# Optimization experiments

Measured on AMD Instinct MI355X. Metric: run time of the kernel, lower is better.

## Reference

```python
import jax, jax.numpy as jnp
import numpy as np

IN_DIM = 128
SLOT_SIZE = 64
NUM_SLOTS = 8
NUM_ITERS = 3
MLP_HDIM = 128
EPSILON = 1e-08


def _layernorm(x, g, b, eps=1e-5):
    m = jnp.mean(x, axis=-1, keepdims=True)
    v = jnp.mean((x - m) ** 2, axis=-1, keepdims=True)
    return (x - m) * jax.lax.rsqrt(v + eps) * g + b


def setup_inputs() -> dict:
    key = jax.random.key(0)
    ks = jax.random.split(key, 16)
    H, D, K, M = SLOT_SIZE, IN_DIM, NUM_SLOTS, MLP_HDIM
    x = jax.random.normal(ks[0], (32, 4096, D), dtype=jnp.float32)
    noise = jax.random.normal(ks[1], (32, K, H), dtype=jnp.float32)
    s = lambda k, shape, fan_in: jax.random.normal(k, shape, jnp.float32) * (1.0 / np.sqrt(fan_in))
    return {
        'x': x,
        'noise': noise,
        'Wq': s(ks[2], (H, H), H),            # project_q (no bias)
        'Wk': s(ks[3], (H, D), D),            # project_k
        'Wv': s(ks[4], (H, D), D),            # project_v
        'ln_in_g': jnp.ones((D,), jnp.float32), 'ln_in_b': jnp.zeros((D,), jnp.float32),
        'ln_sl_g': jnp.ones((H,), jnp.float32), 'ln_sl_b': jnp.zeros((H,), jnp.float32),
        'ln_mlp_g': jnp.ones((H,), jnp.float32), 'ln_mlp_b': jnp.zeros((H,), jnp.float32),
        'gru_w_ih': s(ks[5], (3 * H, H), H),  # PyTorch GRUCell weight_ih (r,z,n)
        'gru_w_hh': s(ks[6], (3 * H, H), H),
        'gru_b_ih': jnp.zeros((3 * H,), jnp.float32),
        'gru_b_hh': jnp.zeros((3 * H,), jnp.float32),
        'mlp_w1': s(ks[7], (M, H), H), 'mlp_b1': jnp.zeros((M,), jnp.float32),
        'mlp_w2': s(ks[8], (H, M), M), 'mlp_b2': jnp.zeros((H,), jnp.float32),
        'slots_mu': jnp.tile(jnp.linspace(-1.0, 1.0, K, dtype=jnp.float32)[None, :, None], (1, 1, H)),
        'slots_logsigma': jnp.full((1, K, H), -1.0, dtype=jnp.float32),
    }


def reference(x, noise, Wq, Wk, Wv, ln_in_g, ln_in_b, ln_sl_g, ln_sl_b,
              ln_mlp_g, ln_mlp_b, gru_w_ih, gru_w_hh, gru_b_ih, gru_b_hh,
              mlp_w1, mlp_b1, mlp_w2, mlp_b2, slots_mu, slots_logsigma):
    B = x.shape[0]
    H, K = SLOT_SIZE, NUM_SLOTS
    xn = _layernorm(x, ln_in_g, ln_in_b)
    k = jnp.einsum('bnd,hd->bnh', xn, Wk)  # [B,N,H]
    v = jnp.einsum('bnd,hd->bnh', xn, Wv)

    scale = jax.nn.softplus(slots_logsigma) + 1e-05
    slots = slots_mu + scale * noise  # rsample, broadcast over batch -> [B,K,H]

    def step(slots):
        slots_prev = slots
        s = _layernorm(slots, ln_sl_g, ln_sl_b)
        q = jnp.einsum('bkh,gh->bkg', s, Wq)  # [B,K,H]
        scores = (H ** -0.5) * jnp.einsum('bnh,bkh->bnk', k, q)
        attn = jax.nn.softmax(scores, axis=-1) + EPSILON  # softmax over slots
        attn = attn / jnp.sum(attn, axis=1, keepdims=True)  # normalize over inputs
        updates = jnp.einsum('bnk,bnh->bkh', attn, v)
        # PyTorch GRUCell: gates ordered (r, z, n)
        u = updates.reshape(-1, H)
        h = slots_prev.reshape(-1, H)
        gx = u @ gru_w_ih.T + gru_b_ih
        gh = h @ gru_w_hh.T + gru_b_hh
        xr, xz, xn_ = jnp.split(gx, 3, axis=-1)
        hr, hz, hn = jnp.split(gh, 3, axis=-1)
        r = jax.nn.sigmoid(xr + hr)
        z = jax.nn.sigmoid(xz + hz)
        n = jnp.tanh(xn_ + r * hn)
        slots = ((1.0 - z) * n + z * h).reshape(B, K, H)
        slots = _layernorm(slots, ln_mlp_g, ln_mlp_b)
        mlp_out = jax.nn.relu(slots @ mlp_w1.T + mlp_b1) @ mlp_w2.T + mlp_b2
        return slots + mlp_out

    for _ in range(NUM_ITERS):
        slots = step(slots)
    return slots
```

## Files before the change

kernel.cpp:

```cpp
#include <hip/hip_runtime.h>

typedef __attribute__((ext_vector_type(8))) short s16x8;
typedef __attribute__((ext_vector_type(4))) float f32x4;

#define DEV static __device__ __forceinline__

DEV float b2f(unsigned short u){
  unsigned int i = ((unsigned int)u) << 16;
  float f; __builtin_memcpy(&f, &i, 4); return f;
}
DEV unsigned short f2b(float f){
  unsigned int i; __builtin_memcpy(&i, &f, 4);
  i = i + 0x7fffu + ((i >> 16) & 1u);
  return (unsigned short)(i >> 16);
}
DEV f32x4 mfma16(s16x8 a, s16x8 b, f32x4 c){
  return __builtin_amdgcn_mfma_f32_16x16x32_bf16(a, b, c, 0, 0, 0);
}
DEV s16x8 ld8f(const float* p){
  const float4* q4 = (const float4*)p;
  float4 a = q4[0], b = q4[1];
  s16x8 r;
  r[0]=(short)f2b(a.x); r[1]=(short)f2b(a.y); r[2]=(short)f2b(a.z); r[3]=(short)f2b(a.w);
  r[4]=(short)f2b(b.x); r[5]=(short)f2b(b.y); r[6]=(short)f2b(b.z); r[7]=(short)f2b(b.w);
  return r;
}

__global__ __launch_bounds__(256) void k_lnkv(
    const float* __restrict__ x,
    const float* __restrict__ Wk,
    const float* __restrict__ Wv,
    const float* __restrict__ lg,
    const float* __restrict__ lb,
    unsigned short* __restrict__ kg,
    unsigned short* __restrict__ vt)
{
  __shared__ unsigned int xs[128 * 68];
  const int tid = threadIdx.x;
  const int w = tid >> 6, ln = tid & 63;
  const int m16 = ln & 15, q = ln >> 4;
  const int b = blockIdx.x >> 5;
  const int nbase = (blockIdx.x & 31) << 7;
  const long rowg0 = (long)b * 4096 + nbase;

  {
    const int half = ln >> 5;
    const int L = ln & 31;
    const float4 gl4 = *(const float4*)(lg + L*4);
    const float4 bl4 = *(const float4*)(lb + L*4);
    for (int i = 0; i < 16; i += 4){
      float4 xv[4];
      #pragma unroll
      for (int j = 0; j < 4; ++j){
        int r = w*32 + (i+j)*2 + half;
        xv[j] = *(const float4*)(x + (rowg0 + r)*128 + L*4);
      }
      #pragma unroll
      for (int j = 0; j < 4; ++j){
        int r = w*32 + (i+j)*2 + half;
        float4 v = xv[j];
        float s1 = v.x + v.y + v.z + v.w;
        float s2 = v.x*v.x + v.y*v.y + v.z*v.z + v.w*v.w;
        #pragma unroll
        for (int m = 16; m >= 1; m >>= 1){
          s1 += __shfl_xor(s1, m);
          s2 += __shfl_xor(s2, m);
        }
        float mean = s1 * (1.f/128.f);
        float var  = s2 * (1.f/128.f) - mean*mean;
        float rs = rsqrtf(var + 1e-5f);
        float y0 = (v.x - mean)*rs*gl4.x + bl4.x;
        float y1 = (v.y - mean)*rs*gl4.y + bl4.y;
        float y2 = (v.z - mean)*rs*gl4.z + bl4.z;
        float y3 = (v.w - mean)*rs*gl4.w + bl4.w;
        uint2 pk;
        pk.x = (unsigned int)f2b(y0) | ((unsigned int)f2b(y1) << 16);
        pk.y = (unsigned int)f2b(y2) | ((unsigned int)f2b(y3) << 16);
        *(uint2*)&xs[r*68 + L*2] = pk;
      }
    }
  }
  __syncthreads();

  s16x8 bw[4][8];
  #pragma unroll
  for (int nt = 0; nt < 8; ++nt){
    const float* Wp = (nt < 4) ? (Wk + (nt*16 + m16)*128)
                               : (Wv + ((nt-4)*16 + m16)*128);
    #pragma unroll
    for (int kb = 0; kb < 4; ++kb)
      bw[kb][nt] = ld8f(Wp + kb*32 + q*8);
  }

  const f32x4 zf = {0.f, 0.f, 0.f, 0.f};
  #pragma unroll
  for (int mi = 0; mi < 2; ++mi){
    int n0 = (w*2 + mi) * 16;
    f32x4 acc[8];
    #pragma unroll
    for (int nt = 0; nt < 8; ++nt) acc[nt] = zf;
    #pragma unroll
    for (int kb = 0; kb < 4; ++kb){
      s16x8 af = *(const s16x8*)((const unsigned short*)(xs + (n0 + m16)*68) + kb*32 + q*8);
      #pragma unroll
      for (int nt = 0; nt < 8; ++nt)
        acc[nt] = mfma16(af, bw[kb][nt], acc[nt]);
    }
    #pragma unroll
    for (int nt = 0; nt < 4; ++nt){
      int h = nt*16 + m16;
      #pragma unroll
      for (int rr = 0; rr < 4; ++rr){
        long n = rowg0 + n0 + q*4 + rr;
        kg[n*64 + h] = f2b(acc[nt][rr]);
      }
    }
    #pragma unroll
    for (int nt = 4; nt < 8; ++nt){
      int h = (nt-4)*16 + m16;
      unsigned int p0 = (unsigned int)f2b(acc[nt][0]) | ((unsigned int)f2b(acc[nt][1]) << 16);
      unsigned int p1 = (unsigned int)f2b(acc[nt][2]) | ((unsigned int)f2b(acc[nt][3]) << 16);
      uint2 pv; pv.x = p0; pv.y = p1;
      long off = ((long)b*64 + h)*4096 + nbase + n0 + q*4;
      *(uint2*)(vt + off) = pv;
    }
  }
}

__global__ __launch_bounds__(256) void k_init2(
    const float* __restrict__ noise,
    const float* __restrict__ mu,
    const float* __restrict__ lsg,
    const float* __restrict__ gsl,
    const float* __restrict__ bsl,
    const float* __restrict__ Wq,
    float* __restrict__ slots,
    unsigned short* __restrict__ qws,
    float* __restrict__ U, float* __restrict__ S)
{
  __shared__ unsigned short st[16*72];
  __shared__ __align__(16) float redS[16][4];
  __shared__ __align__(16) float redQ[16][4];
  const int tid = threadIdx.x;
  const int w = tid >> 6, ln = tid & 63;
  const int m16 = ln & 15, q = ln >> 4;
  const int r0 = blockIdx.x * 16;
  const int cw = w*16 + m16;

  float sl[4], s1[4], s2[4];
  #pragma unroll
  for (int rr = 0; rr < 4; ++rr){
    int row = r0 + q*4 + rr;
    int k = row & 7;
    float v = mu[k*64 + cw] + (log1pf(expf(lsg[k*64 + cw])) + 1e-5f) * noise[row*64 + cw];
    sl[rr] = v;
    slots[row*64 + cw] = v;
    s1[rr] = v; s2[rr] = v*v;
  }
  #pragma unroll
  for (int m = 1; m < 16; m <<= 1){
    #pragma unroll
    for (int rr = 0; rr < 4; ++rr){
      s1[rr] += __shfl_xor(s1[rr], m);
      s2[rr] += __shfl_xor(s2[rr], m);
    }
  }
  if (m16 == 0){
    #pragma unroll
    for (int rr = 0; rr < 4; ++rr){ redS[q*4+rr][w] = s1[rr]; redQ[q*4+rr][w] = s2[rr]; }
  }
  __syncthreads();
  {
    const float gs = gsl[cw], bs = bsl[cw];
    #pragma unroll
    for (int rr = 0; rr < 4; ++rr){
      f32x4 aS = *(const f32x4*)redS[q*4+rr];
      f32x4 aQ = *(const f32x4*)redQ[q*4+rr];
      float tS = aS[0]+aS[1]+aS[2]+aS[3];
      float tQ = aQ[0]+aQ[1]+aQ[2]+aQ[3];
      float mean = tS*(1.f/64.f);
      float var  = tQ*(1.f/64.f) - mean*mean;
      float rs = rsqrtf(var + 1e-5f);
      float sq = (sl[rr] - mean)*rs*gs + bs;
      st[(q*4+rr)*72 + cw] = f2b(sq);
    }
  }
  __syncthreads();
  {
    f32x4 acc = {0,0,0,0};
    #pragma unroll
    for (int ks = 0; ks < 2; ++ks){
      s16x8 a = *(const s16x8*)(st + m16*72 + ks*32 + q*8);
      acc = mfma16(a, ld8f(Wq + cw*64 + ks*32 + q*8), acc);
    }
    #pragma unroll
    for (int rr = 0; rr < 4; ++rr){
      int row = r0 + q*4 + rr;
      int bb_ = row >> 3, kk = row & 7;
      qws[(bb_*16 + kk)*64 + cw] = f2b(acc[rr] * 0.125f);
    }
  }
  {
    f32x4 z = {0,0,0,0};
    *(f32x4*)(U + r0*64 + tid*4) = z;
    if (tid < 16) S[r0 + tid] = 0.f;
    int b0 = blockIdx.x * 2;
    ((unsigned int*)(qws + (b0*16 + 8)*64))[tid] = 0u;
    ((unsigned int*)(qws + ((b0+1)*16 + 8)*64))[tid] = 0u;
  }
}

__global__ __launch_bounds__(256) void k_attn(
    const unsigned short* __restrict__ kg,
    const unsigned short* __restrict__ vt,
    const unsigned short* __restrict__ qws,
    float* __restrict__ U, float* __restrict__ S)
{
  __shared__ float sc[256*17];
  __shared__ unsigned short aT[16*264];
  const int tid = threadIdx.x;
  const int w = tid >> 6, ln = tid & 63;
  const int m16 = ln & 15, q = ln >> 4;
  const int b = blockIdx.x >> 4;
  const int nbase = (blockIdx.x & 15) << 8;

  for (int i = tid; i < 8*264; i += 256) aT[8*264 + i] = 0;

  s16x8 bq[2];
  #pragma unroll
  for (int ks = 0; ks < 2; ++ks)
    bq[ks] = *(const s16x8*)(qws + (b*16 + m16)*64 + ks*32 + q*8);

  #pragma unroll
  for (int mi = 0; mi < 4; ++mi){
    int n0 = (w*4 + mi)*16;
    f32x4 acc = {0.f, 0.f, 0.f, 0.f};
    #pragma unroll
    for (int ks = 0; ks < 2; ++ks){
      s16x8 af = *(const s16x8*)(kg + ((long)b*4096 + nbase + n0 + m16)*64 + ks*32 + q*8);
      acc = mfma16(af, bq[ks], acc);
    }
    #pragma unroll
    for (int rr = 0; rr < 4; ++rr)
      sc[(n0 + q*4 + rr)*17 + m16] = acc[rr];
  }
  __syncthreads();

  {
    int r = tid;
    float a8[8];
    float mx = -1e30f;
    #pragma unroll
    for (int j = 0; j < 8; ++j){ a8[j] = sc[r*17 + j]; mx = fmaxf(mx, a8[j]); }
    float ssum = 0.f;
    #pragma unroll
    for (int j = 0; j < 8; ++j){ a8[j] = expf(a8[j] - mx); ssum += a8[j]; }
    float inv = 1.f/ssum;
    #pragma unroll
    for (int j = 0; j < 8; ++j)
      aT[j*264 + r] = f2b(a8[j]*inv + 1e-8f);
  }
  __syncthreads();

  {
    int j = tid >> 5, c = tid & 31;
    float p = 0.f;
    #pragma unroll
    for (int i = 0; i < 8; ++i) p += b2f(aT[j*264 + c + 32*i]);
    #pragma unroll
    for (int m = 16; m >= 1; m >>= 1) p += __shfl_xor(p, m);
    if ((ln & 31) == 0) atomicAdd(&S[b*8 + j], p);
  }

  {
    f32x4 acc = {0.f, 0.f, 0.f, 0.f};
    #pragma unroll
    for (int ks = 0; ks < 8; ++ks){
      s16x8 af = *(const s16x8*)(aT + m16*264 + ks*32 + q*8);
      s16x8 bf = *(const s16x8*)(vt + ((long)b*64 + w*16 + m16)*4096 + nbase + ks*32 + q*8);
      acc = mfma16(af, bf, acc);
    }
    #pragma unroll
    for (int rr = 0; rr < 4; ++rr){
      int slot = q*4 + rr;
      if (slot < 8)
        atomicAdd(&U[b*512 + slot*64 + w*16 + m16], acc[rr]);
    }
  }
}

__global__ __launch_bounds__(256) void k_gru(
    const float* __restrict__ U, const float* __restrict__ S,
    float* __restrict__ slots,
    const float* __restrict__ wih, const float* __restrict__ whh,
    const float* __restrict__ bih, const float* __restrict__ bhh,
    const float* __restrict__ w1, const float* __restrict__ b1p,
    const float* __restrict__ w2, const float* __restrict__ b2p,
    const float* __restrict__ gmlp, const float* __restrict__ bmlp,
    const float* __restrict__ gsl, const float* __restrict__ bsl,
    const float* __restrict__ Wq,
    unsigned short* __restrict__ qws,
    float* __restrict__ outp,
    float* __restrict__ Uz, float* __restrict__ Sz)
{
  __shared__ unsigned short ut[16*72], ht[16*72], st[16*72], hid[16*136];
  __shared__ __align__(16) float redS[16][4];
  __shared__ __align__(16) float redQ[16][4];
  const int tid = threadIdx.x;
  const int w = tid >> 6, ln = tid & 63;
  const int m16 = ln & 15, q = ln >> 4;
  const int r0 = blockIdx.x * 16;
  const int cw = w*16 + m16;

  #pragma unroll
  for (int p = 0; p < 4; ++p){
    int row = p*4 + w;
    float sv = S[r0 + row];
    float uu = U[(r0 + row)*64 + ln] / sv;
    ut[row*72 + ln] = f2b(uu);
    ht[row*72 + ln] = f2b(slots[(r0 + row)*64 + ln]);
  }
  __syncthreads();

  f32x4 axr = {0,0,0,0}, axz = {0,0,0,0}, axn = {0,0,0,0};
  f32x4 ahr = {0,0,0,0}, ahz = {0,0,0,0}, ahn = {0,0,0,0};
  #pragma unroll
  for (int ks = 0; ks < 2; ++ks){
    s16x8 au = *(const s16x8*)(ut + m16*72 + ks*32 + q*8);
    s16x8 ah = *(const s16x8*)(ht + m16*72 + ks*32 + q*8);
    axr = mfma16(au, ld8f(wih + (      cw)*64 + ks*32 + q*8), axr);
    axz = mfma16(au, ld8f(wih + ( 64 + cw)*64 + ks*32 + q*8), axz);
    axn = mfma16(au, ld8f(wih + (128 + cw)*64 + ks*32 + q*8), axn);
    ahr = mfma16(ah, ld8f(whh + (      cw)*64 + ks*32 + q*8), ahr);
    ahz = mfma16(ah, ld8f(whh + ( 64 + cw)*64 + ks*32 + q*8), ahz);
    ahn = mfma16(ah, ld8f(whh + (128 + cw)*64 + ks*32 + q*8), ahn);
  }
  const float bxr = bih[cw], bxz = bih[64+cw], bxn = bih[128+cw];
  const float bhr = bhh[cw], bhz = bhh[64+cw], bhn = bhh[128+cw];
  float sp[4];
  #pragma unroll
  for (int rr = 0; rr < 4; ++rr){
    float xr = axr[rr] + bxr, xz = axz[rr] + bxz, xnv = axn[rr] + bxn;
    float hr = ahr[rr] + bhr, hz = ahz[rr] + bhz, hn = ahn[rr] + bhn;
    float rg = 1.f / (1.f + expf(-(xr + hr)));
    float zg = 1.f / (1.f + expf(-(xz + hz)));
    float ng = tanhf(xnv + rg*hn);
    float hv = b2f(ht[(q*4 + rr)*72 + cw]);
    sp[rr] = (1.f - zg)*ng + zg*hv;
  }

  float s1[4], s2[4];
  #pragma unroll
  for (int rr = 0; rr < 4; ++rr){ s1[rr] = sp[rr]; s2[rr] = sp[rr]*sp[rr]; }
  #pragma unroll
  for (int m = 1; m < 16; m <<= 1){
    #pragma unroll
    for (int rr = 0; rr < 4; ++rr){
      s1[rr] += __shfl_xor(s1[rr], m);
      s2[rr] += __shfl_xor(s2[rr], m);
    }
  }
  if (m16 == 0){
    #pragma unroll
    for (int rr = 0; rr < 4; ++rr){ redS[q*4+rr][w] = s1[rr]; redQ[q*4+rr][w] = s2[rr]; }
  }
  __syncthreads();
  float sl_[4];
  {
    const float gm = gmlp[cw], bm = bmlp[cw];
    #pragma unroll
    for (int rr = 0; rr < 4; ++rr){
      f32x4 aS = *(const f32x4*)redS[q*4+rr];
      f32x4 aQ = *(const f32x4*)redQ[q*4+rr];
      float tS = aS[0]+aS[1]+aS[2]+aS[3];
      float tQ = aQ[0]+aQ[1]+aQ[2]+aQ[3];
      float mean = tS*(1.f/64.f);
      float var  = tQ*(1.f/64.f) - mean*mean;
      float rs = rsqrtf(var + 1e-5f);
      sl_[rr] = (sp[rr] - mean)*rs*gm + bm;
      st[(q*4+rr)*72 + cw] = f2b(sl_[rr]);
    }
  }
  __syncthreads();

  #pragma unroll
  for (int t2 = 0; t2 < 2; ++t2){
    int nt = w*2 + t2;
    int col = nt*16 + m16;
    f32x4 acc = {0,0,0,0};
    #pragma unroll
    for (int ks = 0; ks < 2; ++ks){
      s16x8 a = *(const s16x8*)(st + m16*72 + ks*32 + q*8);
      acc = mfma16(a, ld8f(w1 + col*64 + ks*32 + q*8), acc);
    }
    float bb = b1p[col];
    #pragma unroll
    for (int rr = 0; rr < 4; ++rr)
      hid[(q*4+rr)*136 + col] = f2b(fmaxf(acc[rr] + bb, 0.f));
  }
  __syncthreads();

  float snew[4];
  {
    f32x4 acc = {0,0,0,0};
    #pragma unroll
    for (int ks = 0; ks < 4; ++ks){
      s16x8 a = *(const s16x8*)(hid + m16*136 + ks*32 + q*8);
      acc = mfma16(a, ld8f(w2 + cw*128 + ks*32 + q*8), acc);
    }
    float bb = b2p[cw];
    #pragma unroll
    for (int rr = 0; rr < 4; ++rr){
      snew[rr] = sl_[rr] + acc[rr] + bb;
      int row = r0 + q*4 + rr;
      slots[row*64 + cw] = snew[rr];
      outp[row*64 + cw] = snew[rr];
    }
  }

  #pragma unroll
  for (int rr = 0; rr < 4; ++rr){ s1[rr] = snew[rr]; s2[rr] = snew[rr]*snew[rr]; }
  #pragma unroll
  for (int m = 1; m < 16; m <<= 1){
    #pragma unroll
    for (int rr = 0; rr < 4; ++rr){
      s1[rr] += __shfl_xor(s1[rr], m);
      s2[rr] += __shfl_xor(s2[rr], m);
    }
  }
  __syncthreads();
  if (m16 == 0){
    #pragma unroll
    for (int rr = 0; rr < 4; ++rr){ redS[q*4+rr][w] = s1[rr]; redQ[q*4+rr][w] = s2[rr]; }
  }
  __syncthreads();
  {
    const float gs = gsl[cw], bs = bsl[cw];
    #pragma unroll
    for (int rr = 0; rr < 4; ++rr){
      f32x4 aS = *(const f32x4*)redS[q*4+rr];
      f32x4 aQ = *(const f32x4*)redQ[q*4+rr];
      float tS = aS[0]+aS[1]+aS[2]+aS[3];
      float tQ = aQ[0]+aQ[1]+aQ[2]+aQ[3];
      float mean = tS*(1.f/64.f);
      float var  = tQ*(1.f/64.f) - mean*mean;
      float rs = rsqrtf(var + 1e-5f);
      float sq = (snew[rr] - mean)*rs*gs + bs;
      st[(q*4+rr)*72 + cw] = f2b(sq);
    }
  }
  __syncthreads();
  {
    f32x4 acc = {0,0,0,0};
    #pragma unroll
    for (int ks = 0; ks < 2; ++ks){
      s16x8 a = *(const s16x8*)(st + m16*72 + ks*32 + q*8);
      acc = mfma16(a, ld8f(Wq + cw*64 + ks*32 + q*8), acc);
    }
    #pragma unroll
    for (int rr = 0; rr < 4; ++rr){
      int row = r0 + q*4 + rr;
      int bb_ = row >> 3, kk = row & 7;
      qws[(bb_*16 + kk)*64 + cw] = f2b(acc[rr] * 0.125f);
    }
  }
  {
    f32x4 z = {0,0,0,0};
    *(f32x4*)(Uz + r0*64 + tid*4) = z;
    if (tid < 16) Sz[r0 + tid] = 0.f;
    int b0 = blockIdx.x * 2;
    unsigned int* qp0 = (unsigned int*)(qws + (b0*16 + 8)*64);
    unsigned int* qp1 = (unsigned int*)(qws + ((b0+1)*16 + 8)*64);
    qp0[tid] = 0u;
    qp1[tid] = 0u;
  }
}

extern "C" void kernel_launch(void* const* d_in, const int* in_sizes, int n_in,
                              void* d_out, int out_size, void* d_ws, size_t ws_size,
                              hipStream_t stream)
{
  const float* x    = (const float*)d_in[0];
  const float* noise= (const float*)d_in[1];
  const float* Wq   = (const float*)d_in[2];
  const float* Wk   = (const float*)d_in[3];
  const float* Wv   = (const float*)d_in[4];
  const float* ling = (const float*)d_in[5];
  const float* linb = (const float*)d_in[6];
  const float* gsl  = (const float*)d_in[7];
  const float* bsl  = (const float*)d_in[8];
  const float* gmlp = (const float*)d_in[9];
  const float* bmlp = (const float*)d_in[10];
  const float* wih  = (const float*)d_in[11];
  const float* whh  = (const float*)d_in[12];
  const float* bih  = (const float*)d_in[13];
  const float* bhh  = (const float*)d_in[14];
  const float* w1   = (const float*)d_in[15];
  const float* b1p  = (const float*)d_in[16];
  const float* w2   = (const float*)d_in[17];
  const float* b2p  = (const float*)d_in[18];
  const float* mu   = (const float*)d_in[19];
  const float* lsg  = (const float*)d_in[20];

  char* ws = (char*)d_ws;
  unsigned short* kg   = (unsigned short*)(ws);
  unsigned short* vt   = (unsigned short*)(ws + 16777216);
  unsigned short* qws  = (unsigned short*)(ws + 33554432);
  float* slots         = (float*)(ws + 33619968);
  float* U             = (float*)(ws + 33685504);
  float* S             = (float*)(ws + 33751040);
  float* outp          = (float*)d_out;

  hipLaunchKernelGGL(k_lnkv, dim3(1024), dim3(256), 0, stream, x, Wk, Wv, ling, linb, kg, vt);
  hipLaunchKernelGGL(k_init2, dim3(16), dim3(256), 0, stream, noise, mu, lsg, gsl, bsl, Wq, slots, qws, U, S);
  for (int it = 0; it < 3; ++it){
    hipLaunchKernelGGL(k_attn, dim3(512), dim3(256), 0, stream, kg, vt, qws, U, S);
    hipLaunchKernelGGL(k_gru, dim3(16), dim3(256), 0, stream, U, S, slots,
                       wih, whh, bih, bhh, w1, b1p, w2, b2p, gmlp, bmlp, gsl, bsl, Wq,
                       qws, outp, U, S);
  }
  (void)in_sizes; (void)n_in; (void)out_size; (void)ws_size;
}
```

Measured before the change: 248.2 us.

## Pre-pack K/V weights to bf16, split projection passes, DPP layernorm reductions

```diff
diff --git a/kernel.cpp b/kernel.cpp
--- a/kernel.cpp
+++ b/kernel.cpp
@@ -26,10 +26,35 @@
   return r;
 }
 
-__global__ __launch_bounds__(256) void k_lnkv(
+template<int C> DEV float dpp_addstep(float x){
+  int y = __builtin_amdgcn_update_dpp(0, __builtin_bit_cast(int, x), C, 0xF, 0xF, true);
+  return x + __builtin_bit_cast(float, y);
+}
+DEV float rsum16(float v){
+  v = dpp_addstep<0xB1>(v);
+  v = dpp_addstep<0x4E>(v);
+  v = dpp_addstep<0x141>(v);
+  v = dpp_addstep<0x140>(v);
+  return v;
+}
+
+__global__ __launch_bounds__(256) void k_wpack(
+    const float* __restrict__ Wk, const float* __restrict__ Wv,
+    unsigned short* __restrict__ wkb, unsigned short* __restrict__ wvb)
+{
+  int t = blockIdx.x * 256 + threadIdx.x;
+  const float* src = (t < 2048) ? (Wk + t*4) : (Wv + (t-2048)*4);
+  unsigned short* dst = (t < 2048) ? (wkb + t*4) : (wvb + (t-2048)*4);
+  float4 v = *(const float4*)src;
+  ushort4 o;
+  o.x = f2b(v.x); o.y = f2b(v.y); o.z = f2b(v.z); o.w = f2b(v.w);
+  *(ushort4*)dst = o;
+}
+
+__global__ __launch_bounds__(256, 4) void k_lnkv(
     const float* __restrict__ x,
-    const float* __restrict__ Wk,
-    const float* __restrict__ Wv,
+    const unsigned short* __restrict__ wkb,
+    const unsigned short* __restrict__ wvb,
     const float* __restrict__ lg,
     const float* __restrict__ lb,
     unsigned short* __restrict__ kg,
@@ -44,82 +69,110 @@
   const long rowg0 = (long)b * 4096 + nbase;
 
   {
-    const int half = ln >> 5;
-    const int L = ln & 31;
-    const float4 gl4 = *(const float4*)(lg + L*4);
-    const float4 bl4 = *(const float4*)(lb + L*4);
-    for (int i = 0; i < 16; i += 4){
-      float4 xv[4];
-      #pragma unroll
-      for (int j = 0; j < 4; ++j){
-        int r = w*32 + (i+j)*2 + half;
-        xv[j] = *(const float4*)(x + (rowg0 + r)*128 + L*4);
+    const int c = m16;
+    const float4 gA = *(const float4*)(lg + c*4);
+    const float4 gB = *(const float4*)(lg + 64 + c*4);
+    const float4 bA = *(const float4*)(lb + c*4);
+    const float4 bB = *(const float4*)(lb + 64 + c*4);
+    const float* base = x + (rowg0 + w*32 + q)*128;
+
+    float4 va[2], vb[2];
+    va[0] = *(const float4*)(base + c*4);
+    vb[0] = *(const float4*)(base + 64 + c*4);
+    #pragma unroll
+    for (int p = 0; p < 8; ++p){
+      const int cur = p & 1, nxt = cur ^ 1;
+      if (p < 7){
+        va[nxt] = *(const float4*)(base + (p+1)*512 + c*4);
+        vb[nxt] = *(const float4*)(base + (p+1)*512 + 64 + c*4);
       }
-      #pragma unroll
-      for (int j = 0; j < 4; ++j){
-        int r = w*32 + (i+j)*2 + half;
-        float4 v = xv[j];
-        float s1 = v.x + v.y + v.z + v.w;
-        float s2 = v.x*v.x + v.y*v.y + v.z*v.z + v.w*v.w;
-        #pragma unroll
-        for (int m = 16; m >= 1; m >>= 1){
-          s1 += __shfl_xor(s1, m);
-          s2 += __shfl_xor(s2, m);
-        }
-        float mean = s1 * (1.f/128.f);
-        float var  = s2 * (1.f/128.f) - mean*mean;
-        float rs = rsqrtf(var + 1e-5f);
-        float y0 = (v.x - mean)*rs*gl4.x + bl4.x;
-        float y1 = (v.y - mean)*rs*gl4.y + bl4.y;
-        float y2 = (v.z - mean)*rs*gl4.z + bl4.z;
-        float y3 = (v.w - mean)*rs*gl4.w + bl4.w;
-        uint2 pk;
-        pk.x = (unsigned int)f2b(y0) | ((unsigned int)f2b(y1) << 16);
-        pk.y = (unsigned int)f2b(y2) | ((unsigned int)f2b(y3) << 16);
-        *(uint2*)&xs[r*68 + L*2] = pk;
-      }
-    }
-  }
-  __syncthreads();
-
-  s16x8 bw[4][8];
-  #pragma unroll
-  for (int nt = 0; nt < 8; ++nt){
-    const float* Wp = (nt < 4) ? (Wk + (nt*16 + m16)*128)
-                               : (Wv + ((nt-4)*16 + m16)*128);
+      float4 u = va[cur], t = vb[cur];
+      float s1 = (u.x + u.y) + (u.z + u.w) + (t.x + t.y) + (t.z + t.w);
+      float s2 = (u.x*u.x + u.y*u.y) + (u.z*u.z + u.w*u.w)
+               + (t.x*t.x + t.y*t.y) + (t.z*t.z + t.w*t.w);
+      s1 = rsum16(s1);
+      s2 = rsum16(s2);
+      float mean = s1 * (1.f/128.f);
+      float var  = s2 * (1.f/128.f) - mean*mean;
+      float rs = rsqrtf(var + 1e-5f);
+      float y0 = (u.x - mean)*rs*gA.x + bA.x;
+      float y1 = (u.y - mean)*rs*gA.y + bA.y;
+      float y2 = (u.z - mean)*rs*gA.z + bA.z;
+      float y3 = (u.w - mean)*rs*gA.w + bA.w;
+      float y4 = (t.x - mean)*rs*gB.x + bB.x;
+      float y5 = (t.y - mean)*rs*gB.y + bB.y;
+      float y6 = (t.z - mean)*rs*gB.z + bB.z;
+      float y7 = (t.w - mean)*rs*gB.w + bB.w;
+      uint2 pkA, pkB;
+      pkA.x = (unsigned int)f2b(y0) | ((unsigned int)f2b(y1) << 16);
+      pkA.y = (unsigned int)f2b(y2) | ((unsigned int)f2b(y3) << 16);
+      pkB.x = (unsigned int)f2b(y4) | ((unsigned int)f2b(y5) << 16);
+      pkB.y = (unsigned int)f2b(y6) | ((unsigned int)f2b(y7) << 16);
+      const int r = w*32 + p*4 + q;
+      *(uint2*)&xs[r*68 + c*2] = pkA;
+      *(uint2*)&xs[r*68 + 32 + c*2] = pkB;
+    }
+  }
+
+  s16x8 bw[4][4];
+  #pragma unroll
+  for (int t = 0; t < 4; ++t)
     #pragma unroll
     for (int kb = 0; kb < 4; ++kb)
-      bw[kb][nt] = ld8f(Wp + kb*32 + q*8);
-  }
+      bw[kb][t] = *(const s16x8*)(wkb + (t*16 + m16)*128 + kb*32 + q*8);
+
+  __syncthreads();
 
   const f32x4 zf = {0.f, 0.f, 0.f, 0.f};
+
   #pragma unroll
   for (int mi = 0; mi < 2; ++mi){
     int n0 = (w*2 + mi) * 16;
-    f32x4 acc[8];
-    #pragma unroll
-    for (int nt = 0; nt < 8; ++nt) acc[nt] = zf;
+    f32x4 acc[4];
+    #pragma unroll
+    for (int t = 0; t < 4; ++t) acc[t] = zf;
     #pragma unroll
     for (int kb = 0; kb < 4; ++kb){
       s16x8 af = *(const s16x8*)((const unsigned short*)(xs + (n0 + m16)*68) + kb*32 + q*8);
       #pragma unroll
-      for (int nt = 0; nt < 8; ++nt)
-        acc[nt] = mfma16(af, bw[kb][nt], acc[nt]);
-    }
-    #pragma unroll
-    for (int nt = 0; nt < 4; ++nt){
-      int h = nt*16 + m16;
+      for (int t = 0; t < 4; ++t)
+        acc[t] = mfma16(af, bw[kb][t], acc[t]);
+    }
+    #pragma unroll
+    for (int t = 0; t < 4; ++t){
+      int h = t*16 + m16;
       #pragma unroll
       for (int rr = 0; rr < 4; ++rr){
         long n = rowg0 + n0 + q*4 + rr;
-        kg[n*64 + h] = f2b(acc[nt][rr]);
+        kg[n*64 + h] = f2b(acc[t][rr]);
       }
     }
-    #pragma unroll
-    for (int nt = 4; nt < 8; ++nt){
-      int h = (nt-4)*16 + m16;
-      unsigned int p0 = (unsigned int)f2b(acc[nt][0]) | ((unsigned int)f2b(acc[nt][1]) << 16);
-      unsigned int p1 = (unsigned int)f2b(acc[nt][2]) | ((unsigned int)f2b(acc[nt][3]) << 16);
+  }
+
+  #pragma unroll
+  for (int t = 0; t < 4; ++t)
+    #pragma unroll
+    for (int kb = 0; kb < 4; ++kb)
+      bw[kb][t] = *(const s16x8*)(wvb + (t*16 + m16)*128 + kb*32 + q*8);
+
+  #pragma unroll
+  for (int mi = 0; mi < 2; ++mi){
+    int n0 = (w*2 + mi) * 16;
+    f32x4 acc[4];
+    #pragma unroll
+    for (int t = 0; t < 4; ++t) acc[t] = zf;
+    #pragma unroll
+    for (int kb = 0; kb < 4; ++kb){
+      s16x8 af = *(const s16x8*)((const unsigned short*)(xs + (n0 + m16)*68) + kb*32 + q*8);
+      #pragma unroll
+      for (int t = 0; t < 4; ++t)
+        acc[t] = mfma16(af, bw[kb][t], acc[t]);
+    }
+    #pragma unroll
+    for (int t = 0; t < 4; ++t){
+      int h = t*16 + m16;
+      unsigned int p0 = (unsigned int)f2b(acc[t][0]) | ((unsigned int)f2b(acc[t][1]) << 16);
+      unsigned int p1 = (unsigned int)f2b(acc[t][2]) | ((unsigned int)f2b(acc[t][3]) << 16);
       uint2 pv; pv.x = p0; pv.y = p1;
       long off = ((long)b*64 + h)*4096 + nbase + n0 + q*4;
       *(uint2*)(vt + off) = pv;
@@ -509,9 +562,12 @@
   float* slots         = (float*)(ws + 33619968);
   float* U             = (float*)(ws + 33685504);
   float* S             = (float*)(ws + 33751040);
+  unsigned short* wkb  = (unsigned short*)(ws + 33752064);
+  unsigned short* wvb  = (unsigned short*)(ws + 33768448);
   float* outp          = (float*)d_out;
 
-  hipLaunchKernelGGL(k_lnkv, dim3(1024), dim3(256), 0, stream, x, Wk, Wv, ling, linb, kg, vt);
+  hipLaunchKernelGGL(k_wpack, dim3(16), dim3(256), 0, stream, Wk, Wv, wkb, wvb);
+  hipLaunchKernelGGL(k_lnkv, dim3(1024), dim3(256), 0, stream, x, wkb, wvb, ling, linb, kg, vt);
   hipLaunchKernelGGL(k_init2, dim3(16), dim3(256), 0, stream, noise, mu, lsg, gsl, bsl, Wq, slots, qws, U, S);
   for (int it = 0; it < 3; ++it){
     hipLaunchKernelGGL(k_attn, dim3(512), dim3(256), 0, stream, kg, vt, qws, U, S);
```

New measurement: 220.0 us. 11.4% less time.
